# Optimization experiments

Measured on AMD Instinct MI355X. Metric: run time of the kernel, lower is better.

## Reference

```python
import jax, jax.numpy as jnp
import numpy as np

HEADS = 16
DIM_HEAD = 64
HEIGHT = 16
KERNEL = 5
DILATION = 1
ALPHA = 32 ** 2


def stable_softmax(t, axis=-1, alpha=ALPHA):
    t = t / alpha
    t = t - jax.lax.stop_gradient(jnp.max(t, axis=axis, keepdims=True))
    return jax.nn.softmax(t * alpha, axis=axis)


def setup_inputs() -> dict:
    key = jax.random.key(0)
    ks = jax.random.split(key, 5)
    b, n, dim = 4, 4097, 1024
    inner = HEADS * DIM_HEAD
    x = jax.random.normal(ks[0], (b, n, dim), dtype=jnp.float32)
    w_qkv = jax.random.normal(ks[1], (dim, 3 * inner), dtype=jnp.float32) * (dim ** -0.5)
    w_out = jax.random.normal(ks[2], (inner, dim), dtype=jnp.float32) * (inner ** -0.5)
    b_out = jax.random.normal(ks[3], (dim,), dtype=jnp.float32) * 0.02
    w_th = jax.random.normal(ks[4], (HEADS, HEADS), dtype=jnp.float32) * (HEADS ** -0.5)
    return {"x": x, "w_qkv": w_qkv, "w_out": w_out, "b_out": b_out, "w_th": w_th}


def reference(x, w_qkv, w_out, b_out, w_th):
    b, n, dim = x.shape
    h, d = HEADS, DIM_HEAD
    height, K, dil = HEIGHT, KERNEL, DILATION
    pad = dil * (K - 1) // 2
    scale = d ** -0.5
    kernel_numel = K * height

    # pad (n-1) non-BOS tokens to a multiple of height (static shapes)
    seq_pad = (-(n - 1)) % height
    xp = jnp.pad(x, ((0, 0), (0, seq_pad), (0, 0))) if seq_pad > 0 else x

    qkv = xp @ w_qkv  # [b, np, 3*inner]
    q, k, v = jnp.split(qkv, 3, axis=-1)

    if n == 1:  # bos-only path
        return v @ w_out + b_out

    out_bos = v[:, :1]  # [b, 1, inner]

    def to_heads(t):
        return t.reshape(b, -1, h, d).transpose(0, 2, 1, 3)  # [b,h,np,d]

    q, k, v = map(to_heads, (q, k, v))
    q = q * scale

    k_bos, k = k[:, :, 0], k[:, :, 1:]
    v_bos, v = v[:, :, 0], v[:, :, 1:]
    q = q[:, :, 1:]

    X = q.shape[2] // height  # number of timesteps

    # k, v as 2D grids [b,h,X,height,d]; unfold local windows along timestep axis
    k = k.reshape(b, h, X, height, d)
    v = v.reshape(b, h, X, height, d)
    kp = jnp.pad(k, ((0, 0), (0, 0), (pad, pad), (0, 0), (0, 0)))
    vp = jnp.pad(v, ((0, 0), (0, 0), (pad, pad), (0, 0), (0, 0)))
    idx = jnp.arange(X)[:, None] + jnp.arange(K)[None, :] * dil  # [X, K]
    kw = kp[:, :, idx].reshape(b, h, X, kernel_numel, d)  # [b,h,X,K*height,d]
    vw = vp[:, :, idx].reshape(b, h, X, kernel_numel, d)

    # prepend BOS key/value to every window
    kb = jnp.broadcast_to(k_bos[:, :, None, None, :], (b, h, X, 1, d))
    vb = jnp.broadcast_to(v_bos[:, :, None, None, :], (b, h, X, 1, d))
    kw = jnp.concatenate([kb, kw], axis=3)  # [b,h,X,1+kn,d]
    vw = jnp.concatenate([vb, vw], axis=3)

    qw = q.reshape(b, h, X, height, d)  # [b,h,X,height,d]
    sim = jnp.einsum('bhnid,bhnjd->bhnij', qw, kw)  # [b,h,X,height,1+kn]

    # causal mask over unfolded windows (BOS column never masked)
    seq_len = X * height
    q_range = jnp.arange(seq_len).reshape(X, height)
    k_range = jnp.pad(jnp.arange(seq_len).reshape(X, height), ((pad, pad), (0, 0)),
                      constant_values=seq_len)
    kr = k_range[idx].reshape(X, kernel_numel)  # [X, kn]
    mask = q_range[:, :, None] < kr[:, None, :]  # [X, height, kn]
    mask = jnp.pad(mask, ((0, 0), (0, 0), (1, 0)), constant_values=False)

    mask_value = -jnp.finfo(sim.dtype).max
    sim = jnp.where(mask[None, None], mask_value, sim)

    attn = stable_softmax(sim, axis=-1)
    # talking heads: 1x1x1 Conv3d over head channels == head mixing matmul
    attn = jnp.einsum('gh,bhnij->bgnij', w_th, attn)

    out = jnp.einsum('bhnij,bhnjd->bhnid', attn, vw)  # [b,h,X,height,d]
    out = out.transpose(0, 2, 3, 1, 4).reshape(b, X * height, h * d)
    out = jnp.concatenate([out_bos, out], axis=1)
    return (out @ w_out + b_out)[:, :n]
```

## Files before the change

### kernel.cpp

```cpp
#include <hip/hip_runtime.h>
#include <stdint.h>

typedef unsigned short u16;
typedef unsigned int u32;
typedef __attribute__((ext_vector_type(8))) short bf16x8;
typedef __attribute__((ext_vector_type(4))) float f32x4;

__device__ __forceinline__ float bf2f(u16 u) {
    union { u32 i; float f; } v; v.i = ((u32)u) << 16; return v.f;
}
__device__ __forceinline__ u16 f2bf(float f) {
    union { float f; u32 i; } v; v.f = f;
    u32 x = v.i;
    u32 r = (x + 0x7FFFu + ((x >> 16) & 1u)) >> 16;
    return (u16)r;
}

__device__ __forceinline__ void gld_lds16(const void* g, void* l) {
    __builtin_amdgcn_global_load_lds(
        (const __attribute__((address_space(1))) void*)g,
        (__attribute__((address_space(3))) void*)l, 16, 0, 0);
}

__global__ __launch_bounds__(256) void cvt_rows(
    const float* __restrict__ src, u16* __restrict__ dst, size_t total4) {
    size_t i = (size_t)blockIdx.x * 256 + threadIdx.x;
    if (i >= total4) return;
    const float4 v = ((const float4*)src)[i];
    u16 o[4] = {f2bf(v.x), f2bf(v.y), f2bf(v.z), f2bf(v.w)};
    *(unsigned long long*)(dst + i * 4) = *(unsigned long long*)o;
}

__global__ __launch_bounds__(256) void transpose_cvt(
    const float* __restrict__ src, u16* __restrict__ dst, int R, int C) {
    __shared__ float tile[32][33];
    int c0 = blockIdx.x * 32, r0 = blockIdx.y * 32;
    int tx = threadIdx.x & 31, ty = threadIdx.x >> 5;
    for (int rr = ty; rr < 32; rr += 8)
        tile[rr][tx] = src[(size_t)(r0 + rr) * C + c0 + tx];
    __syncthreads();
    for (int rr = ty; rr < 32; rr += 8)
        dst[(size_t)(c0 + rr) * R + r0 + tx] = f2bf(tile[tx][rr]);
}

template <int MODE>
__global__ __launch_bounds__(256, 3) void gemm_bt5(
    const u16* __restrict__ A, const u16* __restrict__ Bt,
    const float* __restrict__ bias, void* __restrict__ Cv,
    int M, int N, int K) {
    __shared__ u16 Asb[3][128 * 32];
    __shared__ u16 Bsb[3][128 * 32];
    int tid = threadIdx.x;
    int wid = tid >> 6, lane = tid & 63;
    int lr = lane & 15, lq = lane >> 4;
    int wr = wid >> 1, wc = wid & 1;
    int n0 = blockIdx.x * 128, m0 = blockIdx.y * 128;
    int NT = K >> 5;
    f32x4 acc[4][4] = {};

    #define ST_A(u, t, bi)                                                   \
    do {                                                                     \
        int g = (u) * 256 + tid;                                             \
        int row = g >> 2;                                                    \
        int c = (g & 3) ^ ((row >> 1) & 3);                                  \
        int gm = m0 + row; if (gm >= M) gm = M - 1;                          \
        gld_lds16(A + (size_t)gm * K + ((t) << 5) + c * 8,                   \
                  &Asb[bi][g * 8]);                                          \
    } while (0)
    #define ST_B(u, t, bi)                                                   \
    do {                                                                     \
        int g = (u) * 256 + tid;                                             \
        int row = g >> 2;                                                    \
        int c = (g & 3) ^ ((row >> 1) & 3);                                  \
        gld_lds16(Bt + (size_t)(n0 + row) * K + ((t) << 5) + c * 8,          \
                  &Bsb[bi][g * 8]);                                          \
    } while (0)

    ST_A(0, 0, 0); ST_A(1, 0, 0); ST_B(0, 0, 0); ST_B(1, 0, 0);
    ST_A(0, 1, 1); ST_A(1, 1, 1); ST_B(0, 1, 1); ST_B(1, 1, 1);

    int bcur = 0;
    for (int t = 0; t < NT; ++t) {
        if (t + 1 < NT) asm volatile("s_waitcnt vmcnt(4)" ::: "memory");
        else            asm volatile("s_waitcnt vmcnt(0)" ::: "memory");
        asm volatile("s_barrier" ::: "memory");
        const u16* Ab = &Asb[bcur][0];
        const u16* Bb = &Bsb[bcur][0];
        bf16x8 a[4], b[4];
        #pragma unroll
        for (int mi = 0; mi < 4; ++mi) {
            int r = wr * 64 + mi * 16 + lr;
            int cs = lq ^ ((r >> 1) & 3);
            a[mi] = *(const bf16x8*)&Ab[r * 32 + cs * 8];
        }
        #pragma unroll
        for (int ni = 0; ni < 4; ++ni) {
            int r = wc * 64 + ni * 16 + lr;
            int cs = lq ^ ((r >> 1) & 3);
            b[ni] = *(const bf16x8*)&Bb[r * 32 + cs * 8];
        }
        if (t + 2 < NT) {
            int bst = bcur + 2; if (bst >= 3) bst -= 3;
            ST_A(0, t + 2, bst); ST_A(1, t + 2, bst);
            ST_B(0, t + 2, bst); ST_B(1, t + 2, bst);
        }
        __builtin_amdgcn_s_setprio(1);
        #pragma unroll
        for (int mi = 0; mi < 4; ++mi)
            #pragma unroll
            for (int ni = 0; ni < 4; ++ni)
                acc[mi][ni] = __builtin_amdgcn_mfma_f32_16x16x32_bf16(
                    a[mi], b[ni], acc[mi][ni], 0, 0, 0);
        __builtin_amdgcn_s_setprio(0);
        bcur = bcur + 1; if (bcur == 3) bcur = 0;
    }
    #undef ST_A
    #undef ST_B

    #pragma unroll
    for (int mi = 0; mi < 4; ++mi)
        #pragma unroll
        for (int ni = 0; ni < 4; ++ni) {
            int col = n0 + wc * 64 + ni * 16 + lr;
            float bv = (MODE == 1) ? bias[col] : 0.0f;
            #pragma unroll
            for (int r = 0; r < 4; ++r) {
                int row = m0 + wr * 64 + mi * 16 + lq * 4 + r;
                if (row < M) {
                    if (MODE == 0)
                        ((u16*)Cv)[(size_t)row * N + col] = f2bf(acc[mi][ni][r]);
                    else
                        ((float*)Cv)[(size_t)row * N + col] = acc[mi][ni][r] + bv;
                }
            }
        }
}

__global__ __launch_bounds__(256) void bos_copy(
    const u16* __restrict__ qkv, u16* __restrict__ attn_out) {
    int b = blockIdx.x;
    int c = blockIdx.y * 256 + threadIdx.x;
    attn_out[(size_t)b * 4097 * 1024 + c] =
        qkv[(size_t)b * 4097 * 3072 + 2048 + c];
}

__device__ __forceinline__ int pswz(int j, int i, int h) {
    int byte = j * 512 + i * 32 + h * 2;
    int sw = ((j & 7) ^ ((j >> 3) & 7) ^ ((i >> 2) & 3)) & 7;
    return byte ^ (sw << 4);
}

__global__ __launch_bounds__(256) void attn_kernel(
    const u16* __restrict__ qkv, const float* __restrict__ w_th,
    u16* __restrict__ attn_out) {
    __shared__ u16 P[64 * 16 * 16];
    __shared__ u16 vt[4][2048];
    __shared__ float wth_s[256];

    int tid = threadIdx.x;
    int wid = tid >> 6, lane = tid & 63;
    int x = blockIdx.x;
    int b = blockIdx.y;
    size_t base = (size_t)b * 4097 * 3072;
    int lr = lane & 15;
    int lq = lane >> 4;
    int lk8 = lq * 8;

    wth_s[tid] = w_th[tid];

    for (int hh = 0; hh < 4; ++hh) {
        int h = wid * 4 + hh;
        const u16* qp = qkv + base + (size_t)(1 + x * 16 + lr) * 3072 + h * 64;
        bf16x8 aq0 = *(const bf16x8*)(qp + lk8);
        bf16x8 aq1 = *(const bf16x8*)(qp + 32 + lk8);
        f32x4 acc[4];
        #pragma unroll
        for (int jt = 0; jt < 4; ++jt) {
            int j = jt * 16 + lr;
            int tpos = x * 16 - 32 + (j - 1);
            int t = (j > 0 && tpos >= 0 && tpos < 4096) ? tpos + 1 : 0;
            const u16* kp = qkv + base + (size_t)t * 3072 + 1024 + h * 64;
            bf16x8 bk0 = *(const bf16x8*)(kp + lk8);
            bf16x8 bk1 = *(const bf16x8*)(kp + 32 + lk8);
            f32x4 c = {};
            c = __builtin_amdgcn_mfma_f32_16x16x32_bf16(aq0, bk0, c, 0, 0, 0);
            c = __builtin_amdgcn_mfma_f32_16x16x32_bf16(aq1, bk1, c, 0, 0, 0);
            acc[jt] = c;
        }
        float m[4], s[4], p[4][4];
        #pragma unroll
        for (int r = 0; r < 4; ++r) m[r] = -3.0e38f;
        #pragma unroll
        for (int jt = 0; jt < 4; ++jt) {
            int j = jt * 16 + lr;
            int tpos = x * 16 - 32 + (j - 1);
            bool jvalid = (j == 0) || (tpos >= 0);
            #pragma unroll
            for (int r = 0; r < 4; ++r) {
                int i = lq * 4 + r;
                bool keep = jvalid && (j == 0 || j <= i + 33);
                float v = keep ? acc[jt][r] * 0.125f : -3.0e38f;
                p[jt][r] = v;
                m[r] = fmaxf(m[r], v);
            }
        }
        #pragma unroll
        for (int r = 0; r < 4; ++r) {
            float v = m[r];
            v = fmaxf(v, __shfl_xor(v, 1));
            v = fmaxf(v, __shfl_xor(v, 2));
            v = fmaxf(v, __shfl_xor(v, 4));
            v = fmaxf(v, __shfl_xor(v, 8));
            m[r] = v; s[r] = 0.0f;
        }
        #pragma unroll
        for (int jt = 0; jt < 4; ++jt)
            #pragma unroll
            for (int r = 0; r < 4; ++r) {
                float e = __expf(p[jt][r] - m[r]);
                p[jt][r] = e; s[r] += e;
            }
        #pragma unroll
        for (int r = 0; r < 4; ++r) {
            float v = s[r];
            v += __shfl_xor(v, 1); v += __shfl_xor(v, 2);
            v += __shfl_xor(v, 4); v += __shfl_xor(v, 8);
            s[r] = 1.0f / v;
        }
        #pragma unroll
        for (int jt = 0; jt < 4; ++jt) {
            int j = jt * 16 + lr;
            #pragma unroll
            for (int r = 0; r < 4; ++r) {
                int i = lq * 4 + r;
                *(u16*)((char*)P + pswz(j, i, h)) = f2bf(p[jt][r] * s[r]);
            }
        }
    }
    __syncthreads();

    const u16* vtw = &vt[wid][0];
    int jloc = lane >> 1, dh = lane & 1;
    for (int gg = 0; gg < 4; ++gg) {
        int g = wid * 4 + gg;
        float wth[16];
        #pragma unroll
        for (int h2 = 0; h2 < 16; ++h2) wth[h2] = wth_s[g * 16 + h2];
        f32x4 oacc[4] = {};
        #pragma unroll
        for (int kk = 0; kk < 2; ++kk) {
            {
                int jg = kk * 32 + jloc;
                int tpos = x * 16 - 32 + (jg - 1);
                int t = (jg > 0 && tpos >= 0 && tpos < 4096) ? tpos + 1 : 0;
                const u16* src = qkv + base + (size_t)t * 3072 + 2048 + g * 64
                               + dh * 8;
                #pragma unroll
                for (int w = 0; w < 4; ++w)
                    gld_lds16(src + w * 16, &vt[wid][w * 512 + lane * 8]);
            }
            bf16x8 av;
            #pragma unroll
            for (int e = 0; e < 8; ++e) {
                int j = kk * 32 + lk8 + e;
                bf16x8 v0 = *(const bf16x8*)((const char*)P + pswz(j, lr, 0));
                bf16x8 v1 = *(const bf16x8*)((const char*)P + pswz(j, lr, 8));
                float s0 = 0.0f, s1 = 0.0f;
                #pragma unroll
                for (int h2 = 0; h2 < 8; ++h2) {
                    s0 += wth[h2]     * bf2f((u16)v0[h2]);
                    s1 += wth[h2 + 8] * bf2f((u16)v1[h2]);
                }
                av[e] = (short)f2bf(s0 + s1);
            }
            asm volatile("s_waitcnt vmcnt(0)" ::: "memory");
            #pragma unroll
            for (int dt = 0; dt < 4; ++dt) {
                bf16x8 bv;
                #pragma unroll
                for (int e = 0; e < 8; ++e)
                    bv[e] = (short)vtw[dt * 512 + (lk8 + e) * 16 + lr];
                oacc[dt] = __builtin_amdgcn_mfma_f32_16x16x32_bf16(
                    av, bv, oacc[dt], 0, 0, 0);
            }
        }
        #pragma unroll
        for (int dt = 0; dt < 4; ++dt) {
            int col = g * 64 + dt * 16 + lr;
            #pragma unroll
            for (int r = 0; r < 4; ++r) {
                int i = lq * 4 + r;
                size_t row = (size_t)b * 4097 + 1 + (size_t)x * 16 + i;
                attn_out[row * 1024 + col] = f2bf(oacc[dt][r]);
            }
        }
    }
}

extern "C" void kernel_launch(void* const* d_in, const int* in_sizes, int n_in,
                              void* d_out, int out_size, void* d_ws, size_t ws_size,
                              hipStream_t stream) {
    const float* x     = (const float*)d_in[0];
    const float* w_qkv = (const float*)d_in[1];
    const float* w_out = (const float*)d_in[2];
    const float* b_out = (const float*)d_in[3];
    const float* w_th  = (const float*)d_in[4];
    float* out = (float*)d_out;

    const int M = 4 * 4097;
    u16* qkv      = (u16*)d_ws;
    u16* wqkvT    = qkv + (size_t)M * 3072;
    u16* woutT    = wqkvT + (size_t)3072 * 1024;
    u16* xb       = woutT + (size_t)1024 * 1024;
    u16* attn_out = xb;

    transpose_cvt<<<dim3(96, 32), 256, 0, stream>>>(w_qkv, wqkvT, 1024, 3072);
    transpose_cvt<<<dim3(32, 32), 256, 0, stream>>>(w_out, woutT, 1024, 1024);

    size_t total4 = (size_t)M * 1024 / 4;
    cvt_rows<<<(int)((total4 + 255) / 256), 256, 0, stream>>>(x, xb, total4);

    int mt = (M + 127) / 128;
    gemm_bt5<0><<<dim3(3072 / 128, mt), 256, 0, stream>>>(
        xb, wqkvT, nullptr, qkv, M, 3072, 1024);

    bos_copy<<<dim3(4, 4), 256, 0, stream>>>(qkv, attn_out);
    attn_kernel<<<dim3(256, 4), 256, 0, stream>>>(qkv, w_th, attn_out);

    gemm_bt5<1><<<dim3(1024 / 128, mt), 256, 0, stream>>>(
        attn_out, woutT, b_out, out, M, 1024, 1024);
}
```

Measured before the change: 287.3 us.

## Use larger 128x256 tile GEMM with 512 threads and K=64 stages for QKV projection

Adds a new GEMM kernel with 512 threads per block, a 128x256 output tile and 64-wide K slabs in a triple-buffered LDS pipeline with XOR swizzling, and uses it for the QKV projection. The larger tile raises arithmetic intensity and halves the number of K iterations and barriers. In exchange it uses much more LDS (about 144KB), allows only one block per CU, and launches fewer blocks, which can hurt latency hiding and wave balance.

```diff
diff --git a/kernel.cpp b/kernel.cpp
--- a/kernel.cpp
+++ b/kernel.cpp
@@ -41,6 +41,106 @@
     __syncthreads();
     for (int rr = ty; rr < 32; rr += 8)
         dst[(size_t)(c0 + rr) * R + r0 + tx] = f2bf(tile[tx][rr]);
+}
+
+template <int MODE>
+__global__ __launch_bounds__(512, 1) void gemm_bt6(
+    const u16* __restrict__ A, const u16* __restrict__ Bt,
+    const float* __restrict__ bias, void* __restrict__ Cv,
+    int M, int N, int K) {
+    __shared__ u16 Asb[3][128 * 64];
+    __shared__ u16 Bsb[3][256 * 64];
+    int tid = threadIdx.x;
+    int wid = tid >> 6, lane = tid & 63;
+    int lr = lane & 15, lq = lane >> 4;
+    int wr = wid >> 2, wc = wid & 3;
+    int n0 = blockIdx.x * 256, m0 = blockIdx.y * 128;
+    int NT = K >> 6;
+    f32x4 acc[4][4] = {};
+
+    #define ST_A6(u, t, bi)                                                  \
+    do {                                                                     \
+        int g = (u) * 512 + tid;                                             \
+        int row = g >> 3;                                                    \
+        int c = (g & 7) ^ (row & 7);                                         \
+        int gm = m0 + row; if (gm >= M) gm = M - 1;                          \
+        gld_lds16(A + (size_t)gm * K + ((t) << 6) + c * 8,                   \
+                  &Asb[bi][g * 8]);                                          \
+    } while (0)
+    #define ST_B6(u, t, bi)                                                  \
+    do {                                                                     \
+        int g = (u) * 512 + tid;                                             \
+        int row = g >> 3;                                                    \
+        int c = (g & 7) ^ (row & 7);                                         \
+        gld_lds16(Bt + (size_t)(n0 + row) * K + ((t) << 6) + c * 8,          \
+                  &Bsb[bi][g * 8]);                                          \
+    } while (0)
+
+    ST_A6(0, 0, 0); ST_A6(1, 0, 0);
+    ST_B6(0, 0, 0); ST_B6(1, 0, 0); ST_B6(2, 0, 0); ST_B6(3, 0, 0);
+    ST_A6(0, 1, 1); ST_A6(1, 1, 1);
+    ST_B6(0, 1, 1); ST_B6(1, 1, 1); ST_B6(2, 1, 1); ST_B6(3, 1, 1);
+
+    int bcur = 0;
+    for (int t = 0; t < NT; ++t) {
+        if (t + 1 < NT) asm volatile("s_waitcnt vmcnt(6)" ::: "memory");
+        else            asm volatile("s_waitcnt vmcnt(0)" ::: "memory");
+        asm volatile("s_barrier" ::: "memory");
+        const u16* Ab = &Asb[bcur][0];
+        const u16* Bb = &Bsb[bcur][0];
+        if (t + 2 < NT) {
+            int bst = bcur + 2; if (bst >= 3) bst -= 3;
+            ST_A6(0, t + 2, bst); ST_A6(1, t + 2, bst);
+            ST_B6(0, t + 2, bst); ST_B6(1, t + 2, bst);
+            ST_B6(2, t + 2, bst); ST_B6(3, t + 2, bst);
+        }
+        #pragma unroll
+        for (int ks = 0; ks < 2; ++ks) {
+            bf16x8 a[4], b[4];
+            #pragma unroll
+            for (int mi = 0; mi < 4; ++mi) {
+                int r = wr * 64 + mi * 16 + lr;
+                int cs = (ks * 4 + lq) ^ (r & 7);
+                a[mi] = *(const bf16x8*)&Ab[r * 64 + cs * 8];
+            }
+            #pragma unroll
+            for (int ni = 0; ni < 4; ++ni) {
+                int r = wc * 64 + ni * 16 + lr;
+                int cs = (ks * 4 + lq) ^ (r & 7);
+                b[ni] = *(const bf16x8*)&Bb[r * 64 + cs * 8];
+            }
+            __builtin_amdgcn_s_setprio(1);
+            #pragma unroll
+            for (int mi = 0; mi < 4; ++mi)
+                #pragma unroll
+                for (int ni = 0; ni < 4; ++ni)
+                    acc[mi][ni] = __builtin_amdgcn_mfma_f32_16x16x32_bf16(
+                        a[mi], b[ni], acc[mi][ni], 0, 0, 0);
+            __builtin_amdgcn_s_setprio(0);
+            if (ks == 0) asm volatile("s_barrier" ::: "memory");
+        }
+        bcur = bcur + 1; if (bcur == 3) bcur = 0;
+    }
+    #undef ST_A6
+    #undef ST_B6
+
+    #pragma unroll
+    for (int mi = 0; mi < 4; ++mi)
+        #pragma unroll
+        for (int ni = 0; ni < 4; ++ni) {
+            int col = n0 + wc * 64 + ni * 16 + lr;
+            float bv = (MODE == 1) ? bias[col] : 0.0f;
+            #pragma unroll
+            for (int r = 0; r < 4; ++r) {
+                int row = m0 + wr * 64 + mi * 16 + lq * 4 + r;
+                if (row < M) {
+                    if (MODE == 0)
+                        ((u16*)Cv)[(size_t)row * N + col] = f2bf(acc[mi][ni][r]);
+                    else
+                        ((float*)Cv)[(size_t)row * N + col] = acc[mi][ni][r] + bv;
+                }
+            }
+        }
 }
 
 template <int MODE>
@@ -321,7 +421,7 @@
     cvt_rows<<<(int)((total4 + 255) / 256), 256, 0, stream>>>(x, xb, total4);
 
     int mt = (M + 127) / 128;
-    gemm_bt5<0><<<dim3(3072 / 128, mt), 256, 0, stream>>>(
+    gemm_bt6<0><<<dim3(3072 / 256, mt), 512, 0, stream>>>(
         xb, wqkvT, nullptr, qkv, M, 3072, 1024);
 
     bos_copy<<<dim3(4, 4), 256, 0, stream>>>(qkv, attn_out);
```

Result: slower. 329.7 us (+14.8%).
